# Kernel tuning notes

Measured on AMD Instinct MI355X. Metric: run time of the kernel, lower is better.

Reference implementation:

```python
import jax, jax.numpy as jnp
import numpy as np

N_KPS = 1024      # number of TPS control points
N_PTS = 120000    # number of query points to warp
RELAX = 0.5       # TPS relaxation (regularization on K diagonal)


def setup_inputs() -> dict:
    key = jax.random.key(0)
    k1, k2, k3 = jax.random.split(key, 3)
    # Control points in a [0,100)^2 coordinate frame.
    kps_a = jax.random.uniform(k1, (N_KPS, 2), dtype=jnp.float32) * 100.0
    kps_b = kps_a + jax.random.normal(k2, (N_KPS, 2), dtype=jnp.float32) * 2.0
    # --- replicate __init__: solve the TPS system for W ---
    d2 = jnp.sum((kps_a[:, None, :] - kps_a[None, :, :]) ** 2, axis=-1)  # [n_a, n_a]
    d2 = jnp.where(d2 == 0, 1.0, d2)
    K = 0.5 * d2 * jnp.log(d2) + RELAX * jnp.eye(N_KPS, dtype=jnp.float32)
    P = jnp.concatenate([jnp.ones((N_KPS, 1), jnp.float32), kps_a], axis=1)  # [n_a, 3]
    L = jnp.block([[K, P], [P.T, jnp.zeros((3, 3), jnp.float32)]])           # [n_a+3, n_a+3]
    v = jnp.concatenate([kps_b - kps_a, jnp.zeros((3, 2), jnp.float32)], axis=0)
    W = jnp.linalg.solve(L, v)  # [n_a+3, 2]  (equivalent to L.inverse() @ v)
    # Query points
    pts = jax.random.uniform(k3, (N_PTS, 2), dtype=jnp.float32) * 100.0
    return {"pts": pts, "kps_a": kps_a, "W": W}


def reference(pts, kps_a, W):
    # pairwise squared distances, [n_a, n_b] (matches __build_l2_mat)
    l2 = jnp.sum((kps_a[:, None, :] - pts[None, :, :]) ** 2, axis=-1)
    l2 = jnp.where(l2 == 0, 1.0, l2)
    v = 0.5 * l2 * jnp.log(l2)  # TPS radial basis r^2 * log(r)
    ones = jnp.ones_like(pts[:, 0])
    affine = jnp.stack([ones, pts[:, 0], pts[:, 1]], axis=0)   # [3, n_b]
    x = jnp.concatenate([v, affine], axis=0)                   # [n_a+3, n_b]
    z = x.T @ W                                                # [n_b, 2]
    return pts + z
```

## Files before the change

### kernel.cpp

```cpp
#include <hip/hip_runtime.h>

#define N_KPS 1024
#define N_PTS 120000
#define BLOCK 64

__global__ __launch_bounds__(BLOCK) void tps_warp_kernel(
    const float2* __restrict__ pts,
    const float*  __restrict__ kps,
    const float*  __restrict__ W,
    float2*       __restrict__ out)
{
    const int j = blockIdx.x * BLOCK + threadIdx.x;
    const float2 p = pts[j];

    float zx = 0.0f, zy = 0.0f;

    #pragma unroll 16
    for (int i = 0; i < N_KPS; ++i) {
        float kx = kps[2 * i];
        float ky = kps[2 * i + 1];
        float wx = W[2 * i];
        float wy = W[2 * i + 1];
        float dx = kx - p.x;
        float dy = ky - p.y;
        float d2 = fmaf(dy, dy, dx * dx);
        float t  = __log2f(fmaxf(d2, 1e-37f));
        float v  = d2 * t;
        zx = fmaf(v, wx, zx);
        zy = fmaf(v, wy, zy);
    }

    const float scale = 0.34657359027997264f;

    float w1x = W[2048], w1y = W[2049];
    float wxx = W[2050], wxy = W[2051];
    float wyx = W[2052], wyy = W[2053];

    float ox = p.x + fmaf(scale, zx, fmaf(wxx, p.x, fmaf(wyx, p.y, w1x)));
    float oy = p.y + fmaf(scale, zy, fmaf(wxy, p.x, fmaf(wyy, p.y, w1y)));
    out[j] = make_float2(ox, oy);
}

extern "C" void kernel_launch(void* const* d_in, const int* in_sizes, int n_in,
                              void* d_out, int out_size, void* d_ws, size_t ws_size,
                              hipStream_t stream) {
    const float* pts = (const float*)d_in[0];
    const float* kps = (const float*)d_in[1];
    const float* W   = (const float*)d_in[2];
    float* out = (float*)d_out;

    const int grid = N_PTS / BLOCK;
    tps_warp_kernel<<<grid, BLOCK, 0, stream>>>(
        (const float2*)pts, kps, W, (float2*)out);
}
```

Before: 93.34 us.

## Split keypoint loop across wavefronts and process two points per lane with packed math

Each block now has four wavefronts that each cover a quarter of the control points for the same 128 query points, then combines partial sums through shared memory. Each lane handles two points using 2-wide vector types so the compiler can emit packed FP32 subtract/FMA/mul, and each keypoint/W load is reused across two points. The intent is to cut per-point ALU and load-issue cost and add parallelism. It adds a shared-memory reduction, a barrier, and an idle tail where only one wavefront writes output, and the per-element log2 calls are still scalar.

```diff
diff --git a/kernel.cpp b/kernel.cpp
--- a/kernel.cpp
+++ b/kernel.cpp
@@ -2,7 +2,12 @@
 
 #define N_KPS 1024
 #define N_PTS 120000
-#define BLOCK 64
+#define BLOCK 256
+#define KSPLIT 4
+#define KCHUNK (N_KPS / KSPLIT)
+#define PTS_PER_BLOCK 128
+
+typedef float v2f __attribute__((ext_vector_type(2)));
 
 __global__ __launch_bounds__(BLOCK) void tps_warp_kernel(
     const float2* __restrict__ pts,
@@ -10,35 +15,76 @@
     const float*  __restrict__ W,
     float2*       __restrict__ out)
 {
-    const int j = blockIdx.x * BLOCK + threadIdx.x;
-    const float2 p = pts[j];
+    __shared__ float4 part[KSPLIT][64];
 
-    float zx = 0.0f, zy = 0.0f;
+    const int lane = threadIdx.x & 63;
+    const int kch  = threadIdx.x >> 6;
+    const int base = blockIdx.x * PTS_PER_BLOCK;
+    const int j0 = base + lane;
+    const int j1 = base + 64 + lane;
 
-    #pragma unroll 16
-    for (int i = 0; i < N_KPS; ++i) {
+    const int j0c = j0 < N_PTS ? j0 : N_PTS - 1;
+    const int j1c = j1 < N_PTS ? j1 : N_PTS - 1;
+    const float2 p0 = pts[j0c];
+    const float2 p1 = pts[j1c];
+
+    v2f px = {p0.x, p1.x};
+    v2f py = {p0.y, p1.y};
+    v2f zx = {0.0f, 0.0f};
+    v2f zy = {0.0f, 0.0f};
+    const v2f tiny = {1e-37f, 1e-37f};
+
+    const int k0 = kch * KCHUNK;
+    #pragma unroll 4
+    for (int i = k0; i < k0 + KCHUNK; ++i) {
         float kx = kps[2 * i];
         float ky = kps[2 * i + 1];
         float wx = W[2 * i];
         float wy = W[2 * i + 1];
-        float dx = kx - p.x;
-        float dy = ky - p.y;
-        float d2 = fmaf(dy, dy, dx * dx);
-        float t  = __log2f(fmaxf(d2, 1e-37f));
-        float v  = d2 * t;
-        zx = fmaf(v, wx, zx);
-        zy = fmaf(v, wy, zy);
+        v2f kxv = {kx, kx}, kyv = {ky, ky};
+        v2f wxv = {wx, wx}, wyv = {wy, wy};
+
+        v2f dx = kxv - px;
+        v2f dy = kyv - py;
+        v2f d2 = __builtin_elementwise_fma(dy, dy, dx * dx);
+        d2 = __builtin_elementwise_max(d2, tiny);
+        v2f t;
+        t.x = __log2f(d2.x);
+        t.y = __log2f(d2.y);
+        v2f v = d2 * t;
+        zx = __builtin_elementwise_fma(v, wxv, zx);
+        zy = __builtin_elementwise_fma(v, wyv, zy);
     }
 
-    const float scale = 0.34657359027997264f;
+    part[kch][lane] = make_float4(zx.x, zy.x, zx.y, zy.y);
+    __syncthreads();
 
-    float w1x = W[2048], w1y = W[2049];
-    float wxx = W[2050], wxy = W[2051];
-    float wyx = W[2052], wyy = W[2053];
+    if (kch == 0) {
+        float4 a = part[0][lane];
+        float4 b = part[1][lane];
+        float4 c = part[2][lane];
+        float4 d = part[3][lane];
+        float sx0 = (a.x + b.x) + (c.x + d.x);
+        float sy0 = (a.y + b.y) + (c.y + d.y);
+        float sx1 = (a.z + b.z) + (c.z + d.z);
+        float sy1 = (a.w + b.w) + (c.w + d.w);
 
-    float ox = p.x + fmaf(scale, zx, fmaf(wxx, p.x, fmaf(wyx, p.y, w1x)));
-    float oy = p.y + fmaf(scale, zy, fmaf(wxy, p.x, fmaf(wyy, p.y, w1y)));
-    out[j] = make_float2(ox, oy);
+        const float scale = 0.34657359027997264f;
+        float w1x = W[2048], w1y = W[2049];
+        float wxx = W[2050], wxy = W[2051];
+        float wyx = W[2052], wyy = W[2053];
+
+        if (j0 < N_PTS) {
+            float ox = p0.x + fmaf(scale, sx0, fmaf(wxx, p0.x, fmaf(wyx, p0.y, w1x)));
+            float oy = p0.y + fmaf(scale, sy0, fmaf(wxy, p0.x, fmaf(wyy, p0.y, w1y)));
+            out[j0] = make_float2(ox, oy);
+        }
+        if (j1 < N_PTS) {
+            float ox = p1.x + fmaf(scale, sx1, fmaf(wxx, p1.x, fmaf(wyx, p1.y, w1x)));
+            float oy = p1.y + fmaf(scale, sy1, fmaf(wxy, p1.x, fmaf(wyy, p1.y, w1y)));
+            out[j1] = make_float2(ox, oy);
+        }
+    }
 }
 
 extern "C" void kernel_launch(void* const* d_in, const int* in_sizes, int n_in,
@@ -49,7 +95,7 @@
     const float* W   = (const float*)d_in[2];
     float* out = (float*)d_out;
 
-    const int grid = N_PTS / BLOCK;
+    const int grid = (N_PTS + PTS_PER_BLOCK - 1) / PTS_PER_BLOCK;
     tps_warp_kernel<<<grid, BLOCK, 0, stream>>>(
         (const float2*)pts, kps, W, (float2*)out);
 }
```

Result: faster. 88.39 us (-5.3%).

## Split keypoint loop across four waves with packed-float2 math and LDS reduction

Applied to the files above, without the earlier changes.

Each block now holds four waves that share the same 64 query points, with each wave processing a quarter of the control points, and the partial sums are combined through shared memory. A small setup kernel rearranges keypoints and weights into a structure-of-arrays float2 layout so the inner loop can use packed two-wide FMA/sub/max operations. The goal is more parallelism per point (4x more waves in flight) and fewer VALU instructions per pair. In exchange it adds an extra kernel launch, a block barrier, and leaves three waves idle during the epilogue.

```diff
diff --git a/kernel.cpp b/kernel.cpp
--- a/kernel.cpp
+++ b/kernel.cpp
@@ -2,43 +2,94 @@
 
 #define N_KPS 1024
 #define N_PTS 120000
-#define BLOCK 64
+#define BLOCK 256
+#define KSPLIT 4
+#define NGROUPS (N_KPS / 2)
+#define GPW (NGROUPS / KSPLIT)
+
+typedef float v2f __attribute__((ext_vector_type(2)));
+
+__global__ __launch_bounds__(512) void tps_setup_kernel(
+    const float* __restrict__ kps,
+    const float* __restrict__ W,
+    float2*      __restrict__ ws)
+{
+    const int t = threadIdx.x;
+    float2 kx = make_float2(kps[4 * t],     kps[4 * t + 2]);
+    float2 ky = make_float2(kps[4 * t + 1], kps[4 * t + 3]);
+    float2 wx = make_float2(W[4 * t],       W[4 * t + 2]);
+    float2 wy = make_float2(W[4 * t + 1],   W[4 * t + 3]);
+    ws[t]             = kx;
+    ws[512 + t]       = ky;
+    ws[1024 + t]      = wx;
+    ws[1536 + t]      = wy;
+}
 
 __global__ __launch_bounds__(BLOCK) void tps_warp_kernel(
     const float2* __restrict__ pts,
-    const float*  __restrict__ kps,
     const float*  __restrict__ W,
+    const float2* __restrict__ ws,
     float2*       __restrict__ out)
 {
-    const int j = blockIdx.x * BLOCK + threadIdx.x;
+    __shared__ float2 part[KSPLIT][64];
+
+    const int lane = threadIdx.x & 63;
+    const int wv = __builtin_amdgcn_readfirstlane(threadIdx.x) >> 6;
+
+    const int j = blockIdx.x * 64 + lane;
     const float2 p = pts[j];
 
-    float zx = 0.0f, zy = 0.0f;
+    const v2f px = {p.x, p.x};
+    const v2f py = {p.y, p.y};
+    const v2f tiny = {1e-37f, 1e-37f};
+    v2f zx = {0.0f, 0.0f};
+    v2f zy = {0.0f, 0.0f};
 
-    #pragma unroll 16
-    for (int i = 0; i < N_KPS; ++i) {
-        float kx = kps[2 * i];
-        float ky = kps[2 * i + 1];
-        float wx = W[2 * i];
-        float wy = W[2 * i + 1];
-        float dx = kx - p.x;
-        float dy = ky - p.y;
-        float d2 = fmaf(dy, dy, dx * dx);
-        float t  = __log2f(fmaxf(d2, 1e-37f));
-        float v  = d2 * t;
-        zx = fmaf(v, wx, zx);
-        zy = fmaf(v, wy, zy);
+    const float2* __restrict__ KX = ws;
+    const float2* __restrict__ KY = ws + 512;
+    const float2* __restrict__ WX = ws + 1024;
+    const float2* __restrict__ WY = ws + 1536;
+
+    const int g0 = wv * GPW;
+    #pragma unroll 8
+    for (int g = g0; g < g0 + GPW; ++g) {
+        float2 kx = KX[g];
+        float2 ky = KY[g];
+        float2 wx = WX[g];
+        float2 wy = WY[g];
+
+        v2f dx = v2f{kx.x, kx.y} - px;
+        v2f dy = v2f{ky.x, ky.y} - py;
+        v2f d2 = __builtin_elementwise_fma(dy, dy, dx * dx);
+        d2 = __builtin_elementwise_max(d2, tiny);
+        v2f t;
+        t.x = __log2f(d2.x);
+        t.y = __log2f(d2.y);
+        v2f v = d2 * t;
+        zx = __builtin_elementwise_fma(v, v2f{wx.x, wx.y}, zx);
+        zy = __builtin_elementwise_fma(v, v2f{wy.x, wy.y}, zy);
     }
 
-    const float scale = 0.34657359027997264f;
+    part[wv][lane] = make_float2(zx.x + zx.y, zy.x + zy.y);
+    __syncthreads();
 
-    float w1x = W[2048], w1y = W[2049];
-    float wxx = W[2050], wxy = W[2051];
-    float wyx = W[2052], wyy = W[2053];
+    if (wv == 0) {
+        float2 a = part[0][lane];
+        float2 b = part[1][lane];
+        float2 c = part[2][lane];
+        float2 d = part[3][lane];
+        float sx = (a.x + b.x) + (c.x + d.x);
+        float sy = (a.y + b.y) + (c.y + d.y);
 
-    float ox = p.x + fmaf(scale, zx, fmaf(wxx, p.x, fmaf(wyx, p.y, w1x)));
-    float oy = p.y + fmaf(scale, zy, fmaf(wxy, p.x, fmaf(wyy, p.y, w1y)));
-    out[j] = make_float2(ox, oy);
+        const float scale = 0.34657359027997264f;
+        float w1x = W[2048], w1y = W[2049];
+        float wxx = W[2050], wxy = W[2051];
+        float wyx = W[2052], wyy = W[2053];
+
+        float ox = p.x + fmaf(scale, sx, fmaf(wxx, p.x, fmaf(wyx, p.y, w1x)));
+        float oy = p.y + fmaf(scale, sy, fmaf(wxy, p.x, fmaf(wyy, p.y, w1y)));
+        out[j] = make_float2(ox, oy);
+    }
 }
 
 extern "C" void kernel_launch(void* const* d_in, const int* in_sizes, int n_in,
@@ -48,8 +99,11 @@
     const float* kps = (const float*)d_in[1];
     const float* W   = (const float*)d_in[2];
     float* out = (float*)d_out;
+    float2* ws = (float2*)d_ws;
 
-    const int grid = N_PTS / BLOCK;
+    tps_setup_kernel<<<1, 512, 0, stream>>>(kps, W, ws);
+
+    const int grid = N_PTS / 64;
     tps_warp_kernel<<<grid, BLOCK, 0, stream>>>(
-        (const float2*)pts, kps, W, (float2*)out);
+        (const float2*)pts, W, (const float2*)ws, (float2*)out);
 }
```

Result: faster. 84.38 us (-9.6%).

## Split control-point loop across four waves with LDS reduction and raw log2

Applied to the files above, without the earlier changes.

Each block now serves 64 points with four wavefronts, each summing a quarter of the control points, and the partial sums are combined through shared memory. The goal is four times as many waves in flight, which helps with only 1875 original blocks on a many-CU GPU. The log is switched to the raw hardware log2 builtin, and the clamp is folded into an fma epsilon so the max instruction disappears. The cost is a barrier plus an LDS reduction per block, with three of the four waves idle at the end.

```diff
diff --git a/kernel.cpp b/kernel.cpp
--- a/kernel.cpp
+++ b/kernel.cpp
@@ -2,7 +2,15 @@
 
 #define N_KPS 1024
 #define N_PTS 120000
-#define BLOCK 64
+#define BLOCK 256
+#define KSPLIT 4
+#define KCHUNK (N_KPS / KSPLIT)
+
+#if __has_builtin(__builtin_amdgcn_logf)
+#define RAW_LOG2(x) __builtin_amdgcn_logf(x)
+#else
+#define RAW_LOG2(x) __log2f(x)
+#endif
 
 __global__ __launch_bounds__(BLOCK) void tps_warp_kernel(
     const float2* __restrict__ pts,
@@ -10,35 +18,53 @@
     const float*  __restrict__ W,
     float2*       __restrict__ out)
 {
-    const int j = blockIdx.x * BLOCK + threadIdx.x;
+    __shared__ float2 part[KSPLIT][64];
+
+    const int lane = threadIdx.x & 63;
+    const int wv = __builtin_amdgcn_readfirstlane(threadIdx.x) >> 6;
+
+    const int j = blockIdx.x * 64 + lane;
     const float2 p = pts[j];
 
     float zx = 0.0f, zy = 0.0f;
 
-    #pragma unroll 16
-    for (int i = 0; i < N_KPS; ++i) {
+    const int i0 = wv * KCHUNK;
+    #pragma unroll 8
+    for (int i = i0; i < i0 + KCHUNK; ++i) {
         float kx = kps[2 * i];
         float ky = kps[2 * i + 1];
         float wx = W[2 * i];
         float wy = W[2 * i + 1];
+
         float dx = kx - p.x;
         float dy = ky - p.y;
-        float d2 = fmaf(dy, dy, dx * dx);
-        float t  = __log2f(fmaxf(d2, 1e-37f));
+        float d2 = fmaf(dy, dy, fmaf(dx, dx, 1e-37f));
+        float t  = RAW_LOG2(d2);
         float v  = d2 * t;
         zx = fmaf(v, wx, zx);
         zy = fmaf(v, wy, zy);
     }
 
-    const float scale = 0.34657359027997264f;
+    part[wv][lane] = make_float2(zx, zy);
+    __syncthreads();
 
-    float w1x = W[2048], w1y = W[2049];
-    float wxx = W[2050], wxy = W[2051];
-    float wyx = W[2052], wyy = W[2053];
+    if (wv == 0) {
+        float2 a = part[0][lane];
+        float2 b = part[1][lane];
+        float2 c = part[2][lane];
+        float2 d = part[3][lane];
+        float sx = (a.x + b.x) + (c.x + d.x);
+        float sy = (a.y + b.y) + (c.y + d.y);
 
-    float ox = p.x + fmaf(scale, zx, fmaf(wxx, p.x, fmaf(wyx, p.y, w1x)));
-    float oy = p.y + fmaf(scale, zy, fmaf(wxy, p.x, fmaf(wyy, p.y, w1y)));
-    out[j] = make_float2(ox, oy);
+        const float scale = 0.34657359027997264f;
+        float w1x = W[2048], w1y = W[2049];
+        float wxx = W[2050], wxy = W[2051];
+        float wyx = W[2052], wyy = W[2053];
+
+        float ox = p.x + fmaf(scale, sx, fmaf(wxx, p.x, fmaf(wyx, p.y, w1x)));
+        float oy = p.y + fmaf(scale, sy, fmaf(wxy, p.x, fmaf(wyy, p.y, w1y)));
+        out[j] = make_float2(ox, oy);
+    }
 }
 
 extern "C" void kernel_launch(void* const* d_in, const int* in_sizes, int n_in,
@@ -49,7 +75,7 @@
     const float* W   = (const float*)d_in[2];
     float* out = (float*)d_out;
 
-    const int grid = N_PTS / BLOCK;
+    const int grid = N_PTS / 64;
     tps_warp_kernel<<<grid, BLOCK, 0, stream>>>(
         (const float2*)pts, kps, W, (float2*)out);
 }
```

Result: faster. 85.29 us (-8.6%).
